# Kernel tuning notes

Measured on AMD Instinct MI355X. Metric: run time of the kernel, lower is better.

The kernel has to match this reference:

```python
import jax, jax.numpy as jnp
import numpy as np

B, T, H = 32, 2048, 1024


def setup_inputs() -> dict:
    key = jax.random.key(0)
    ks = jax.random.split(key, 5)
    s = 1.0 / np.sqrt(H)
    return {
        "x": jax.random.normal(ks[0], (B, H), dtype=jnp.float32),
        "context": jax.random.normal(ks[1], (B, T, H), dtype=jnp.float32),
        "mask": jnp.ones((B, T), dtype=bool),
        "Wq": jax.random.normal(ks[2], (H, H), dtype=jnp.float32) * s,
        "bq": jnp.zeros((H,), dtype=jnp.float32),
        "Wm": jax.random.normal(ks[3], (H, H), dtype=jnp.float32) * s,
        "bm": jnp.zeros((H,), dtype=jnp.float32),
        "v": jax.random.normal(ks[4], (H,), dtype=jnp.float32) * s,
    }


def reference(x, context, mask, Wq, bq, Wm, bm, v):
    # h_x: [B,1,H]; h_c: [B,T,H]  (mask is unused, matching the original module)
    h_x = (x @ Wq.T + bq)[:, None, :]
    h_c = jnp.einsum('bth,oh->bto', context, Wm) + bm
    # score: [B,T] = tanh(h_x + h_c) . v, then softmax over T
    score = jax.nn.softmax(jnp.einsum('bth,h->bt', jnp.tanh(h_x + h_c), v), axis=-1)
    # context-weighted sum over T -> [B,H]
    c = jnp.einsum('bth,bt->bh', context, score)
    return (c, score)
```

## Files before the change

### kernel.cpp

```cpp
#include <hip/hip_runtime.h>
#include <math.h>

#define B_ 32
#define T_ 2048
#define H_ 1024

typedef __bf16 bf16x8 __attribute__((ext_vector_type(8)));
typedef float f32x4 __attribute__((ext_vector_type(4)));

__device__ __forceinline__ unsigned short f2bf(float f) {
  unsigned int u = __float_as_uint(f);
  u += 0x7fffu + ((u >> 16) & 1u);
  return (unsigned short)(u >> 16);
}

__device__ __forceinline__ float fast_tanh(float x) {
  float e = __expf(2.0f * x);
  return 1.0f - __fdividef(2.0f, e + 1.0f);
}

__device__ __forceinline__ void async16(const void* g, void* l) {
  typedef const __attribute__((address_space(1))) void* gvp;
  typedef __attribute__((address_space(3))) void* lvp;
  __builtin_amdgcn_global_load_lds((gvp)(unsigned long long)g,
                                   (lvp)(unsigned int)(unsigned long long)l,
                                   16, 0, 0);
}

__global__ void prep_kernel(const float* __restrict__ x, const float* __restrict__ Wq,
                            const float* __restrict__ bq, const float* __restrict__ bm,
                            const float* __restrict__ Wm,
                            float* __restrict__ hxb, unsigned short* __restrict__ wmb,
                            float* __restrict__ logits, float* __restrict__ outc) {
  int blk = blockIdx.x, tid = threadIdx.x;
  if (blk < 8192) {
    int wave = tid >> 6, lane = tid & 63;
    int pair = (blk << 2) + wave;
    int b = pair >> 10, o = pair & (H_ - 1);
    const float4* wr = (const float4*)(Wq + (size_t)o * H_);
    const float4* xr = (const float4*)(x + (size_t)b * H_);
    float s = 0.f;
#pragma unroll
    for (int s4 = 0; s4 < 4; ++s4) {
      float4 wv = wr[(s4 << 6) + lane];
      float4 xv = xr[(s4 << 6) + lane];
      s += wv.x * xv.x + wv.y * xv.y + wv.z * xv.z + wv.w * xv.w;
    }
#pragma unroll
    for (int d = 1; d < 64; d <<= 1) s += __shfl_xor(s, d);
    if (lane == 0) hxb[(b << 10) + o] = s + bq[o] + bm[o];
  } else if (blk < 9216) {
    int i = ((blk - 8192) << 10) + (tid << 2);
    float4 wv = *(const float4*)(Wm + i);
    *(ushort4*)(wmb + i) = make_ushort4(f2bf(wv.x), f2bf(wv.y), f2bf(wv.z), f2bf(wv.w));
  } else if (blk < 9280) {
    int zb = blk - 9216;
    *(float4*)(logits + (zb << 10) + (tid << 2)) = (float4){0.f, 0.f, 0.f, 0.f};
  } else {
    int zb = blk - 9280;
    *(float4*)(outc + (zb << 10) + (tid << 2)) = (float4){0.f, 0.f, 0.f, 0.f};
  }
}

__global__ __launch_bounds__(256) void score_kernel(
    const float* __restrict__ ctx, const unsigned short* __restrict__ wmb,
    const float* __restrict__ hxb, const float* __restrict__ v,
    float* __restrict__ logits) {
  __shared__ __align__(16) unsigned short As[128 * 64];
  __shared__ __align__(16) unsigned short Bs[128 * 64];
  __shared__ float part[128];

  int tid = threadIdx.x;
  int bx = blockIdx.x;
  int g = bx >> 3;
  int oc = bx & 7;
  int b = g >> 4;
  int t0 = (g & 15) << 7;
  int o0 = oc << 7;
  if (tid < 128) part[tid] = 0.f;

  int lane = tid & 63;
  int wave = tid >> 6;
  int wm = (wave >> 1) << 6;
  int wn = (wave & 1) << 6;
  int q = lane >> 4;
  int m = lane & 15;

  const float* cf = ctx + ((size_t)b * T_ + t0) * H_;
  const unsigned short* wb = wmb + (size_t)o0 * H_;

  f32x4 acc[4][4];
#pragma unroll
  for (int i = 0; i < 4; ++i)
#pragma unroll
    for (int j = 0; j < 4; ++j) acc[i][j] = (f32x4){0.f, 0.f, 0.f, 0.f};

  for (int k0 = 0; k0 < H_; k0 += 64) {
    __syncthreads();
#pragma unroll
    for (int i = 0; i < 4; ++i) {
      int ig = (wave << 2) + i;
      int p = (ig << 6) + lane;
      int row = p >> 3;
      int gl = (p & 7) ^ (row & 7);
      size_t goff = (size_t)row * H_ + k0 + (gl << 3);
      async16(wb + goff, (char*)Bs + ((size_t)ig << 10));
      int arow = (tid >> 3) + (i << 5);
      int agl = tid & 7;
      int agp = agl ^ (arow & 7);
      const float* src = cf + (size_t)arow * H_ + k0 + (agl << 3);
      float4 f0 = *(const float4*)(src);
      float4 f1 = *(const float4*)(src + 4);
      unsigned short* dst = As + (arow << 6) + (agp << 3);
      *(ushort4*)(dst) = make_ushort4(f2bf(f0.x), f2bf(f0.y), f2bf(f0.z), f2bf(f0.w));
      *(ushort4*)(dst + 4) = make_ushort4(f2bf(f1.x), f2bf(f1.y), f2bf(f1.z), f2bf(f1.w));
    }
    __syncthreads();
#pragma unroll
    for (int kk = 0; kk < 2; ++kk) {
      bf16x8 af[4], bfr[4];
#pragma unroll
      for (int i = 0; i < 4; ++i) {
        int row = wm + (i << 4) + m;
        int gp = ((kk << 2) + q) ^ (row & 7);
        af[i] = *(const bf16x8*)(As + (row << 6) + (gp << 3));
      }
#pragma unroll
      for (int j = 0; j < 4; ++j) {
        int row = wn + (j << 4) + m;
        int gp = ((kk << 2) + q) ^ (row & 7);
        bfr[j] = *(const bf16x8*)(Bs + (row << 6) + (gp << 3));
      }
#pragma unroll
      for (int i = 0; i < 4; ++i)
#pragma unroll
        for (int j = 0; j < 4; ++j)
          acc[i][j] = __builtin_amdgcn_mfma_f32_16x16x32_bf16(af[i], bfr[j], acc[i][j], 0, 0, 0);
    }
  }

  float hb[4], vv[4];
#pragma unroll
  for (int j = 0; j < 4; ++j) {
    int o = o0 + wn + (j << 4) + m;
    hb[j] = hxb[(b << 10) + o];
    vv[j] = v[o];
  }
#pragma unroll
  for (int i = 0; i < 4; ++i) {
#pragma unroll
    for (int r = 0; r < 4; ++r) {
      float s = 0.f;
#pragma unroll
      for (int j = 0; j < 4; ++j) s += fast_tanh(acc[i][j][r] + hb[j]) * vv[j];
      s += __shfl_xor(s, 1);
      s += __shfl_xor(s, 2);
      s += __shfl_xor(s, 4);
      s += __shfl_xor(s, 8);
      if (m == 0) atomicAdd(&part[wm + (i << 4) + (q << 2) + r], s);
    }
  }
  __syncthreads();
  if (tid < 128) atomicAdd(&logits[b * T_ + t0 + tid], part[tid]);
}

__global__ void wsum_kernel(const float* __restrict__ ctx,
                            const float* __restrict__ logits,
                            float* __restrict__ score, float* __restrict__ outc) {
  int tid = threadIdx.x;
  int b = blockIdx.y;
  int tc = blockIdx.x << 6;
  __shared__ float wred[4];
  __shared__ float sc[64];

  const float* lb = logits + b * T_;
  float l[8];
  float mx = -3.4e38f;
#pragma unroll
  for (int i = 0; i < 8; ++i) { l[i] = lb[tid + (i << 8)]; mx = fmaxf(mx, l[i]); }
#pragma unroll
  for (int d = 1; d < 64; d <<= 1) mx = fmaxf(mx, __shfl_xor(mx, d));
  if ((tid & 63) == 0) wred[tid >> 6] = mx;
  __syncthreads();
  mx = fmaxf(fmaxf(wred[0], wred[1]), fmaxf(wred[2], wred[3]));
  __syncthreads();
  float e[8];
  float se = 0.f;
#pragma unroll
  for (int i = 0; i < 8; ++i) { e[i] = __expf(l[i] - mx); se += e[i]; }
#pragma unroll
  for (int d = 1; d < 64; d <<= 1) se += __shfl_xor(se, d);
  if ((tid & 63) == 0) wred[tid >> 6] = se;
  __syncthreads();
  se = wred[0] + wred[1] + wred[2] + wred[3];
  float inv = 1.0f / se;
#pragma unroll
  for (int i = 0; i < 8; ++i) {
    int tg = tid + (i << 8);
    if ((tg >> 6) == (int)blockIdx.x) sc[tg & 63] = e[i] * inv;
  }
  if (blockIdx.x == 0) {
#pragma unroll
    for (int i = 0; i < 8; ++i) score[b * T_ + tid + (i << 8)] = e[i] * inv;
  }
  __syncthreads();

  int h = tid << 2;
  const float* cp = ctx + ((size_t)b * T_ + tc) * H_ + h;
  float s0 = 0.f, s1 = 0.f, s2 = 0.f, s3 = 0.f;
#pragma unroll 4
  for (int t = 0; t < 64; ++t) {
    float4 f = *(const float4*)(cp + (size_t)t * H_);
    float w = sc[t];
    s0 += f.x * w; s1 += f.y * w; s2 += f.z * w; s3 += f.w * w;
  }
  float* op = outc + (b << 10) + h;
  atomicAdd(op + 0, s0);
  atomicAdd(op + 1, s1);
  atomicAdd(op + 2, s2);
  atomicAdd(op + 3, s3);
}

extern "C" void kernel_launch(void* const* d_in, const int* in_sizes, int n_in,
                              void* d_out, int out_size, void* d_ws, size_t ws_size,
                              hipStream_t stream) {
  const float* x   = (const float*)d_in[0];
  const float* ctx = (const float*)d_in[1];
  const float* Wq  = (const float*)d_in[3];
  const float* bq  = (const float*)d_in[4];
  const float* Wm  = (const float*)d_in[5];
  const float* bm  = (const float*)d_in[6];
  const float* v   = (const float*)d_in[7];

  float* out_c = (float*)d_out;
  float* out_s = out_c + B_ * H_;

  char* ws = (char*)d_ws;
  float* hxb = (float*)ws;
  unsigned short* wmb = (unsigned short*)(ws + 131072);
  float* logits = (float*)(ws + 131072 + 2097152);

  prep_kernel<<<dim3(9312), 256, 0, stream>>>(x, Wq, bq, bm, Wm, hxb, wmb,
                                              logits, out_c);
  score_kernel<<<dim3(4096), 256, 0, stream>>>(ctx, wmb, hxb, v, logits);
  wsum_kernel<<<dim3(T_ / 64, B_), 256, 0, stream>>>(ctx, logits, out_s, out_c);
}
```

Before: 706.5 us.

## Stage fp32 context via async LDS loads, reorder blocks, coarsen prep and wsum

The score kernel now copies fp32 context tiles straight into LDS with global_load_lds and converts them to bf16 while building the MFMA fragments. This replaces the per-thread global load, convert and LDS store, at the cost of doubling A-tile LDS usage. The block index is remapped so the o-tile is the outer index, which changes how Wm and context tiles are shared in L2. The prep kernel reuses each Wq row across all batches with far fewer blocks, and the weighted-sum kernel processes 128 timesteps per block, halving its atomics.

```diff
diff --git a/kernel.cpp b/kernel.cpp
--- a/kernel.cpp
+++ b/kernel.cpp
@@ -33,50 +33,63 @@
                             float* __restrict__ hxb, unsigned short* __restrict__ wmb,
                             float* __restrict__ logits, float* __restrict__ outc) {
   int blk = blockIdx.x, tid = threadIdx.x;
-  if (blk < 8192) {
+  if (blk < 256) {
     int wave = tid >> 6, lane = tid & 63;
-    int pair = (blk << 2) + wave;
-    int b = pair >> 10, o = pair & (H_ - 1);
+    int o = (blk << 2) + wave;
     const float4* wr = (const float4*)(Wq + (size_t)o * H_);
-    const float4* xr = (const float4*)(x + (size_t)b * H_);
-    float s = 0.f;
-#pragma unroll
-    for (int s4 = 0; s4 < 4; ++s4) {
-      float4 wv = wr[(s4 << 6) + lane];
-      float4 xv = xr[(s4 << 6) + lane];
-      s += wv.x * xv.x + wv.y * xv.y + wv.z * xv.z + wv.w * xv.w;
-    }
-#pragma unroll
-    for (int d = 1; d < 64; d <<= 1) s += __shfl_xor(s, d);
-    if (lane == 0) hxb[(b << 10) + o] = s + bq[o] + bm[o];
-  } else if (blk < 9216) {
-    int i = ((blk - 8192) << 10) + (tid << 2);
-    float4 wv = *(const float4*)(Wm + i);
-    *(ushort4*)(wmb + i) = make_ushort4(f2bf(wv.x), f2bf(wv.y), f2bf(wv.z), f2bf(wv.w));
-  } else if (blk < 9280) {
-    int zb = blk - 9216;
-    *(float4*)(logits + (zb << 10) + (tid << 2)) = (float4){0.f, 0.f, 0.f, 0.f};
+    float4 wv[4];
+#pragma unroll
+    for (int s4 = 0; s4 < 4; ++s4) wv[s4] = wr[(s4 << 6) + lane];
+    float bias = bq[o] + bm[o];
+#pragma unroll 4
+    for (int b = 0; b < B_; ++b) {
+      const float4* xr = (const float4*)(x + (size_t)b * H_);
+      float s = 0.f;
+#pragma unroll
+      for (int s4 = 0; s4 < 4; ++s4) {
+        float4 xv = xr[(s4 << 6) + lane];
+        s += wv[s4].x * xv.x + wv[s4].y * xv.y + wv[s4].z * xv.z + wv[s4].w * xv.w;
+      }
+#pragma unroll
+      for (int d = 1; d < 64; d <<= 1) s += __shfl_xor(s, d);
+      if (lane == 0) hxb[(b << 10) + o] = s + bias;
+    }
+  } else if (blk < 512) {
+    int i0 = ((blk - 256) << 12) + (tid << 2);
+#pragma unroll
+    for (int it = 0; it < 4; ++it) {
+      int i = i0 + (it << 10);
+      float4 wv = *(const float4*)(Wm + i);
+      *(ushort4*)(wmb + i) = make_ushort4(f2bf(wv.x), f2bf(wv.y), f2bf(wv.z), f2bf(wv.w));
+    }
+  } else if (blk < 528) {
+    int i0 = ((blk - 512) << 12) + (tid << 2);
+#pragma unroll
+    for (int it = 0; it < 4; ++it)
+      *(float4*)(logits + i0 + (it << 10)) = (float4){0.f, 0.f, 0.f, 0.f};
   } else {
-    int zb = blk - 9280;
-    *(float4*)(outc + (zb << 10) + (tid << 2)) = (float4){0.f, 0.f, 0.f, 0.f};
+    int i0 = ((blk - 528) << 12) + (tid << 2);
+#pragma unroll
+    for (int it = 0; it < 4; ++it)
+      *(float4*)(outc + i0 + (it << 10)) = (float4){0.f, 0.f, 0.f, 0.f};
   }
 }
 
 __global__ __launch_bounds__(256) void score_kernel(
     const float* __restrict__ ctx, const unsigned short* __restrict__ wmb,
     const float* __restrict__ hxb, const float* __restrict__ v,
-    float* __restrict__ logits) {
-  __shared__ __align__(16) unsigned short As[128 * 64];
+    float* logits) {
+  __shared__ __align__(16) float As[128 * 64];
   __shared__ __align__(16) unsigned short Bs[128 * 64];
   __shared__ float part[128];
 
   int tid = threadIdx.x;
-  int bx = blockIdx.x;
-  int g = bx >> 3;
-  int oc = bx & 7;
-  int b = g >> 4;
-  int t0 = (g & 15) << 7;
-  int o0 = oc << 7;
+  int xx = blockIdx.x;
+  int ot = xx >> 9;
+  int bt = xx & 511;
+  int b = bt >> 4;
+  int t0 = (bt & 15) << 7;
+  int o0 = ot << 7;
   if (tid < 128) part[tid] = 0.f;
 
   int lane = tid & 63;
@@ -97,6 +110,16 @@
 
   for (int k0 = 0; k0 < H_; k0 += 64) {
     __syncthreads();
+#pragma unroll
+    for (int i = 0; i < 8; ++i) {
+      int ig = (wave << 3) + i;
+      int p = (ig << 6) + lane;
+      int row = p >> 4;
+      int pg = p & 15;
+      int lg = (pg & 8) | ((pg & 7) ^ (row & 7));
+      size_t goff = (size_t)row * H_ + k0 + (lg << 2);
+      async16(cf + goff, (char*)As + ((size_t)ig << 10));
+    }
 #pragma unroll
     for (int i = 0; i < 4; ++i) {
       int ig = (wave << 2) + i;
@@ -105,15 +128,6 @@
       int gl = (p & 7) ^ (row & 7);
       size_t goff = (size_t)row * H_ + k0 + (gl << 3);
       async16(wb + goff, (char*)Bs + ((size_t)ig << 10));
-      int arow = (tid >> 3) + (i << 5);
-      int agl = tid & 7;
-      int agp = agl ^ (arow & 7);
-      const float* src = cf + (size_t)arow * H_ + k0 + (agl << 3);
-      float4 f0 = *(const float4*)(src);
-      float4 f1 = *(const float4*)(src + 4);
-      unsigned short* dst = As + (arow << 6) + (agp << 3);
-      *(ushort4*)(dst) = make_ushort4(f2bf(f0.x), f2bf(f0.y), f2bf(f0.z), f2bf(f0.w));
-      *(ushort4*)(dst + 4) = make_ushort4(f2bf(f1.x), f2bf(f1.y), f2bf(f1.z), f2bf(f1.w));
     }
     __syncthreads();
 #pragma unroll
@@ -122,8 +136,18 @@
 #pragma unroll
       for (int i = 0; i < 4; ++i) {
         int row = wm + (i << 4) + m;
-        int gp = ((kk << 2) + q) ^ (row & 7);
-        af[i] = *(const bf16x8*)(As + (row << 6) + (gp << 3));
+        int lg0 = ((kk << 2) + q) << 1;
+        int ph0 = (lg0 & 8) | ((lg0 & 7) ^ (row & 7));
+        int lg1 = lg0 | 1;
+        int ph1 = (lg1 & 8) | ((lg1 & 7) ^ (row & 7));
+        f32x4 a0 = *(const f32x4*)(As + (row << 6) + (ph0 << 2));
+        f32x4 a1 = *(const f32x4*)(As + (row << 6) + (ph1 << 2));
+        bf16x8 t;
+        t[0] = (__bf16)a0[0]; t[1] = (__bf16)a0[1];
+        t[2] = (__bf16)a0[2]; t[3] = (__bf16)a0[3];
+        t[4] = (__bf16)a1[0]; t[5] = (__bf16)a1[1];
+        t[6] = (__bf16)a1[2]; t[7] = (__bf16)a1[3];
+        af[i] = t;
       }
 #pragma unroll
       for (int j = 0; j < 4; ++j) {
@@ -169,9 +193,9 @@
                             float* __restrict__ score, float* __restrict__ outc) {
   int tid = threadIdx.x;
   int b = blockIdx.y;
-  int tc = blockIdx.x << 6;
+  int tc = blockIdx.x << 7;
   __shared__ float wred[4];
-  __shared__ float sc[64];
+  __shared__ float sc[128];
 
   const float* lb = logits + b * T_;
   float l[8];
@@ -197,7 +221,7 @@
 #pragma unroll
   for (int i = 0; i < 8; ++i) {
     int tg = tid + (i << 8);
-    if ((tg >> 6) == (int)blockIdx.x) sc[tg & 63] = e[i] * inv;
+    if ((tg >> 7) == (int)blockIdx.x) sc[tg & 127] = e[i] * inv;
   }
   if (blockIdx.x == 0) {
 #pragma unroll
@@ -209,7 +233,7 @@
   const float* cp = ctx + ((size_t)b * T_ + tc) * H_ + h;
   float s0 = 0.f, s1 = 0.f, s2 = 0.f, s3 = 0.f;
 #pragma unroll 4
-  for (int t = 0; t < 64; ++t) {
+  for (int t = 0; t < 128; ++t) {
     float4 f = *(const float4*)(cp + (size_t)t * H_);
     float w = sc[t];
     s0 += f.x * w; s1 += f.y * w; s2 += f.z * w; s3 += f.w * w;
@@ -240,8 +264,8 @@
   unsigned short* wmb = (unsigned short*)(ws + 131072);
   float* logits = (float*)(ws + 131072 + 2097152);
 
-  prep_kernel<<<dim3(9312), 256, 0, stream>>>(x, Wq, bq, bm, Wm, hxb, wmb,
-                                              logits, out_c);
+  prep_kernel<<<dim3(536), 256, 0, stream>>>(x, Wq, bq, bm, Wm, hxb, wmb,
+                                             logits, out_c);
   score_kernel<<<dim3(4096), 256, 0, stream>>>(ctx, wmb, hxb, v, logits);
-  wsum_kernel<<<dim3(T_ / 64, B_), 256, 0, stream>>>(ctx, logits, out_s, out_c);
-}
+  wsum_kernel<<<dim3(T_ / 128, B_), 256, 0, stream>>>(ctx, logits, out_s, out_c);
+}
```

New measurement: 728.4 us. +3.1%, slower.
